# Optimization experiments

Hardware: AMD Instinct MI355X
Metric: run time of the kernel (lower is better)

Reference implementation:

```python
import jax, jax.numpy as jnp
import numpy as np
import math

D_MODEL = 1024
N_HEADS = 16
HEAD_DIM = D_MODEL // N_HEADS


def setup_inputs() -> dict:
    key = jax.random.key(0)
    k1, k2, k3 = jax.random.split(key, 3)
    B, T = 2, 2048
    x = jax.random.normal(k1, (B, T, D_MODEL), dtype=jnp.float32)
    W_qkv = jax.random.normal(k2, (D_MODEL, 3 * D_MODEL), dtype=jnp.float32) * (1.0 / math.sqrt(D_MODEL))
    W_out = jax.random.normal(k3, (D_MODEL, D_MODEL), dtype=jnp.float32) * (1.0 / math.sqrt(D_MODEL))
    return {"x": x, "W_qkv": W_qkv, "W_out": W_out}


def reference(x, W_qkv, W_out):
    B, T, C = x.shape
    qkv = x @ W_qkv  # [B, T, 3C]
    q, k, v = jnp.split(qkv, 3, axis=-1)

    def heads(t):  # [B,T,C] -> [B,H,T,Dh]
        return t.reshape(B, T, N_HEADS, HEAD_DIM).transpose(0, 2, 1, 3)

    q, k, v = heads(q), heads(k), heads(v)
    scale = 1.0 / math.sqrt(HEAD_DIM)
    scores = jnp.einsum('bhtd,bhsd->bhts', q, k) * scale  # [B,H,T,T]
    causal = jnp.tril(jnp.ones((T, T), dtype=bool))
    scores = jnp.where(causal[None, None, :, :], scores, -jnp.inf)
    attn = jax.nn.softmax(scores, axis=-1)
    out = jnp.einsum('bhts,bhsd->bhtd', attn, v)  # [B,H,T,Dh]
    out = out.transpose(0, 2, 1, 3).reshape(B, T, C)
    return out @ W_out
```

## Files before the change

kernel.cpp:

```cpp
#include <hip/hip_runtime.h>
#include <hip/hip_bf16.h>

typedef __bf16 bf16;
typedef bf16 bf16x4 __attribute__((ext_vector_type(4)));
typedef bf16 bf16x8 __attribute__((ext_vector_type(8)));
typedef float f32x4 __attribute__((ext_vector_type(4)));

#define GLOAD16(g, l) __builtin_amdgcn_global_load_lds( \
    (const __attribute__((address_space(1))) void*)(g),  \
    (__attribute__((address_space(3))) void*)(l), 16, 0, 0)

#define EXP2F(x) __builtin_amdgcn_exp2f(x)
#define MFMA16(a, b, c) __builtin_amdgcn_mfma_f32_16x16x32_bf16(a, b, c, 0, 0, 0)

__global__ __launch_bounds__(256) void prep(const float* __restrict__ x,
                                            const float* __restrict__ Wqkv,
                                            const float* __restrict__ Wout,
                                            bf16* __restrict__ xb,
                                            bf16* __restrict__ wqkvT,
                                            bf16* __restrict__ woutT) {
  int id = blockIdx.x, tid = threadIdx.x;
  if (id < 2048) {
    int i = id * 256 + tid;
    const float4* p = (const float4*)x + (size_t)i * 2;
    float4 a = p[0], b = p[1];
    bf16x8 o;
    o[0] = (bf16)a.x; o[1] = (bf16)a.y; o[2] = (bf16)a.z; o[3] = (bf16)a.w;
    o[4] = (bf16)b.x; o[5] = (bf16)b.y; o[6] = (bf16)b.z; o[7] = (bf16)b.w;
    ((bf16x8*)xb)[i] = o;
  } else {
    __shared__ float tile[32][33];
    const float* src; bf16* dst; int N, j;
    if (id < 5120) { src = Wqkv; dst = wqkvT; N = 3072; j = id - 2048; }
    else           { src = Wout; dst = woutT; N = 1024; j = id - 5120; }
    int ntile = N / 32;
    int n0 = (j % ntile) * 32, k0 = (j / ntile) * 32;
    int tx = tid & 31, ty = tid >> 5;
#pragma unroll
    for (int i = 0; i < 4; i++)
      tile[ty + 8 * i][tx] = src[(size_t)(k0 + ty + 8 * i) * N + n0 + tx];
    __syncthreads();
#pragma unroll
    for (int i = 0; i < 4; i++)
      dst[(size_t)(n0 + ty + 8 * i) * 1024 + k0 + tx] = (bf16)tile[tx][ty + 8 * i];
  }
}

__device__ __forceinline__ void gemm_mainloop64(const bf16* __restrict__ A,
                                                const bf16* __restrict__ Bt,
                                                int K, int m0, int n0,
                                                f32x4 acc[4][4],
                                                bf16* As, bf16* Bs) {
  int tid = threadIdx.x;
  int lane = tid & 63;
  int wave = tid >> 6;
  int wr = wave >> 1, wc = wave & 1;
  int c16 = lane & 15, g = lane >> 4;
  f32x4 z = {0.f, 0.f, 0.f, 0.f};
#pragma unroll
  for (int m = 0; m < 4; m++)
#pragma unroll
    for (int n = 0; n < 4; n++) acc[m][n] = z;
  for (int k0 = 0; k0 < K; k0 += 64) {
#pragma unroll
    for (int i = 0; i < 4; i++) {
      int cc = tid + i * 256;
      int r = cc >> 3, ch = cc & 7;
      int sc = ch ^ (r & 7);
      GLOAD16(A + (size_t)(m0 + r) * K + k0 + sc * 8, As + cc * 8);
    }
#pragma unroll
    for (int i = 0; i < 4; i++) {
      int cc = tid + i * 256;
      int r = cc >> 3, ch = cc & 7;
      int sc = ch ^ (r & 7);
      GLOAD16(Bt + (size_t)(n0 + r) * K + k0 + sc * 8, Bs + cc * 8);
    }
    __syncthreads();
#pragma unroll
    for (int h = 0; h < 2; h++) {
      bf16x8 af[4], bfr[4];
#pragma unroll
      for (int m = 0; m < 4; m++) {
        int ar = wr * 64 + m * 16 + c16;
        af[m] = *(const bf16x8*)((const char*)As + ar * 128 + (((h * 4 + g) ^ (ar & 7)) << 4));
      }
#pragma unroll
      for (int n = 0; n < 4; n++) {
        int br = wc * 64 + n * 16 + c16;
        bfr[n] = *(const bf16x8*)((const char*)Bs + br * 128 + (((h * 4 + g) ^ (br & 7)) << 4));
      }
      __builtin_amdgcn_s_setprio(1);
#pragma unroll
      for (int m = 0; m < 4; m++)
#pragma unroll
        for (int n = 0; n < 4; n++)
          acc[m][n] = MFMA16(af[m], bfr[n], acc[m][n]);
      __builtin_amdgcn_s_setprio(0);
    }
    __syncthreads();
  }
}

__global__ __launch_bounds__(256) void gemm_qkv(const bf16* __restrict__ A,
                                                const bf16* __restrict__ Bt,
                                                bf16* __restrict__ q,
                                                bf16* __restrict__ kk,
                                                bf16* __restrict__ vt) {
  __shared__ bf16 As[128 * 64];
  __shared__ bf16 Bs[128 * 64];
  int id = blockIdx.x;
  int xc = id & 7, k = id >> 3;
  int bn = xc * 3 + (k % 3), bm = k / 3;
  int m0 = bm * 128, n0 = bn * 128;
  f32x4 acc[4][4];
  gemm_mainloop64(A, Bt, 1024, m0, n0, acc, As, Bs);
  int lane = threadIdx.x & 63;
  int wave = threadIdx.x >> 6;
  int wr = wave >> 1, wc = wave & 1;
  int c16 = lane & 15, g = lane >> 4;
  int which = n0 >> 10;
  const float QSCALE = 0.125f * 1.4426950408889634f;
  if (which == 2) {
#pragma unroll
    for (int m = 0; m < 4; m++)
#pragma unroll
      for (int n = 0; n < 4; n++) {
        int gm0 = m0 + wr * 64 + m * 16 + g * 4;
        int gn = n0 + wc * 64 + n * 16 + c16;
        int rem = gn & 1023, h = rem >> 6, d = rem & 63;
        int b = gm0 >> 11, t0 = gm0 & 2047;
        size_t bh = (size_t)(b * 16 + h);
        bf16x4 pv;
        pv[0] = (bf16)acc[m][n][0]; pv[1] = (bf16)acc[m][n][1];
        pv[2] = (bf16)acc[m][n][2]; pv[3] = (bf16)acc[m][n][3];
        *(bf16x4*)(vt + (bh * 64 + d) * 2048 + t0) = pv;
      }
  } else {
#pragma unroll
    for (int m = 0; m < 4; m++)
#pragma unroll
      for (int n = 0; n < 4; n++)
#pragma unroll
        for (int j = 0; j < 4; j++) {
          int gm = m0 + wr * 64 + m * 16 + g * 4 + j;
          int gn = n0 + wc * 64 + n * 16 + c16;
          int rem = gn & 1023, h = rem >> 6, d = rem & 63;
          int b = gm >> 11, t = gm & 2047;
          float v = acc[m][n][j];
          size_t bh = (size_t)(b * 16 + h);
          if (which == 0) q[(bh * 2048 + t) * 64 + d]  = (bf16)(v * QSCALE);
          else            kk[(bh * 2048 + t) * 64 + d] = (bf16)v;
        }
  }
}

__global__ __launch_bounds__(256) void gemm_out(const bf16* __restrict__ A,
                                                const bf16* __restrict__ Bt,
                                                float* __restrict__ C) {
  __shared__ bf16 As[64 * 64];
  __shared__ bf16 Bs[128 * 64];
  int tid = threadIdx.x;
  int lane = tid & 63;
  int wave = tid >> 6;
  int wr = wave >> 1, wc = wave & 1;
  int c16 = lane & 15, g = lane >> 4;
  int id = blockIdx.x;
  int bn = id & 7, bm = id >> 3;
  int m0 = bm * 64, n0 = bn * 128;
  const int K = 1024;
  f32x4 acc[2][4];
  {
    f32x4 z = {0.f, 0.f, 0.f, 0.f};
#pragma unroll
    for (int m = 0; m < 2; m++)
#pragma unroll
      for (int n = 0; n < 4; n++) acc[m][n] = z;
  }
  for (int k0 = 0; k0 < K; k0 += 64) {
#pragma unroll
    for (int i = 0; i < 2; i++) {
      int cc = tid + i * 256;
      int r = cc >> 3, ch = cc & 7;
      int sc = ch ^ (r & 7);
      GLOAD16(A + (size_t)(m0 + r) * K + k0 + sc * 8, As + cc * 8);
    }
#pragma unroll
    for (int i = 0; i < 4; i++) {
      int cc = tid + i * 256;
      int r = cc >> 3, ch = cc & 7;
      int sc = ch ^ (r & 7);
      GLOAD16(Bt + (size_t)(n0 + r) * K + k0 + sc * 8, Bs + cc * 8);
    }
    __syncthreads();
#pragma unroll
    for (int h = 0; h < 2; h++) {
      bf16x8 af[2], bfr[4];
#pragma unroll
      for (int m = 0; m < 2; m++) {
        int ar = wr * 32 + m * 16 + c16;
        af[m] = *(const bf16x8*)((const char*)As + ar * 128 + (((h * 4 + g) ^ (ar & 7)) << 4));
      }
#pragma unroll
      for (int n = 0; n < 4; n++) {
        int br = wc * 64 + n * 16 + c16;
        bfr[n] = *(const bf16x8*)((const char*)Bs + br * 128 + (((h * 4 + g) ^ (br & 7)) << 4));
      }
      __builtin_amdgcn_s_setprio(1);
#pragma unroll
      for (int m = 0; m < 2; m++)
#pragma unroll
        for (int n = 0; n < 4; n++)
          acc[m][n] = MFMA16(af[m], bfr[n], acc[m][n]);
      __builtin_amdgcn_s_setprio(0);
    }
    __syncthreads();
  }
#pragma unroll
  for (int m = 0; m < 2; m++)
#pragma unroll
    for (int n = 0; n < 4; n++)
#pragma unroll
      for (int j = 0; j < 4; j++) {
        int gm = m0 + wr * 32 + m * 16 + g * 4 + j;
        int gn = n0 + wc * 64 + n * 16 + c16;
        C[(size_t)gm * 1024 + gn] = acc[m][n][j];
      }
}

__global__ __launch_bounds__(256) void attn(const bf16* __restrict__ q,
                                            const bf16* __restrict__ kk,
                                            const bf16* __restrict__ vt,
                                            bf16* __restrict__ out) {
  __shared__ bf16 Ks[4][64 * 64];
  __shared__ bf16 Vs[4][64 * 64];
  __shared__ bf16 Ps[4 * 32 * 64];
  int tid = threadIdx.x, lane = tid & 63, w = tid >> 6;
  int c16 = lane & 15, g = (lane >> 4) & 3, g4 = g * 4;

  int id = blockIdx.x;
  int c = id & 7;
  int k = id >> 3;
  int s = k >> 5;
  int j5 = k & 31;
  int bxi = j5 & 15, b2 = j5 >> 4;
  int bx = s ? (15 - bxi) : bxi;
  int bh = 4 * c + 2 * b2 + s;
  int q0 = bx * 128;

  const bf16* qb = q  + (size_t)bh * 2048 * 64;
  const bf16* kb = kk + (size_t)bh * 2048 * 64;
  const bf16* vb = vt + (size_t)bh * 64 * 2048;
  int nt = 2 * bx + 2;
  int ns = nt >> 1;

  int qlo = q0 + w * 32;
  bf16x8 qf[2][2];
#pragma unroll
  for (int m = 0; m < 2; m++)
#pragma unroll
    for (int ks = 0; ks < 2; ks++)
      qf[m][ks] = *(const bf16x8*)(qb + (size_t)(qlo + m * 16 + c16) * 64 + ks * 32 + g * 8);
#pragma unroll
  for (int i = 0; i < 2; i++) {
    int cc = tid + i * 256;
    int r = cc >> 3;
    int sw = ((cc & 7) ^ (r & 7)) * 8;
    GLOAD16(kb + (size_t)r * 64 + sw, Ks[0] + cc * 8);
    GLOAD16(vb + (size_t)r * 2048 + sw, Vs[0] + cc * 8);
    GLOAD16(kb + (size_t)(64 + r) * 64 + sw, Ks[1] + cc * 8);
    GLOAD16(vb + (size_t)r * 2048 + 64 + sw, Vs[1] + cc * 8);
  }
  __syncthreads();

  f32x4 o[2][4];
  float lrun[2] = {0.f, 0.f};
  {
    f32x4 z = {0.f, 0.f, 0.f, 0.f};
#pragma unroll
    for (int m = 0; m < 2; m++)
#pragma unroll
      for (int n = 0; n < 4; n++) o[m][n] = z;
  }
  bf16* Pw = Ps + w * 2048;

  for (int st = 0; st < ns; ++st) {
    if (st + 1 < ns) {
      int sn = st * 128 + 128;
      int nb = (2 * st + 2) & 3;
#pragma unroll
      for (int i = 0; i < 2; i++) {
        int cc = tid + i * 256;
        int r = cc >> 3;
        int sw = ((cc & 7) ^ (r & 7)) * 8;
        GLOAD16(kb + (size_t)(sn + r) * 64 + sw, Ks[nb] + cc * 8);
        GLOAD16(vb + (size_t)r * 2048 + sn + sw, Vs[nb] + cc * 8);
        GLOAD16(kb + (size_t)(sn + 64 + r) * 64 + sw, Ks[nb + 1] + cc * 8);
        GLOAD16(vb + (size_t)r * 2048 + sn + 64 + sw, Vs[nb + 1] + cc * 8);
      }
    }
#pragma unroll
    for (int half = 0; half < 2; ++half) {
      int t = 2 * st + half;
      int s0 = t * 64;
      if (s0 > qlo + 31) continue;
      const char* Kb = (const char*)Ks[t & 3];
      const char* Vb = (const char*)Vs[t & 3];
      f32x4 S[2][4];
      {
        f32x4 z = {0.f, 0.f, 0.f, 0.f};
#pragma unroll
        for (int m = 0; m < 2; m++)
#pragma unroll
          for (int n = 0; n < 4; n++) S[m][n] = z;
      }
      __builtin_amdgcn_s_setprio(1);
#pragma unroll
      for (int ks = 0; ks < 2; ks++) {
        bf16x8 kf[4];
#pragma unroll
        for (int n = 0; n < 4; n++) {
          int srow = n * 16 + c16;
          kf[n] = *(const bf16x8*)(Kb + srow * 128 + (((ks * 4 + g) ^ (srow & 7)) << 4));
        }
#pragma unroll
        for (int m = 0; m < 2; m++)
#pragma unroll
          for (int n = 0; n < 4; n++)
            S[m][n] = MFMA16(kf[n], qf[m][ks], S[m][n]);
      }
      __builtin_amdgcn_s_setprio(0);
      bool diag = (s0 + 63 > qlo);
#pragma unroll
      for (int m = 0; m < 2; m++) {
        int qr = qlo + m * 16 + c16;
        if (diag) {
#pragma unroll
          for (int n = 0; n < 4; n++)
#pragma unroll
            for (int rr = 0; rr < 4; rr++)
              if (s0 + n * 16 + g4 + rr > qr) S[m][n][rr] = -__builtin_inff();
        }
        float p[4][4];
        float rs = 0.f;
#pragma unroll
        for (int n = 0; n < 4; n++)
#pragma unroll
          for (int rr = 0; rr < 4; rr++) {
            p[n][rr] = EXP2F(S[m][n][rr]);
            rs += p[n][rr];
          }
        lrun[m] += rs;
        int rp = m * 16 + c16;
#pragma unroll
        for (int n = 0; n < 4; n++) {
          bf16x4 pw;
          pw[0] = (bf16)p[n][0]; pw[1] = (bf16)p[n][1];
          pw[2] = (bf16)p[n][2]; pw[3] = (bf16)p[n][3];
          *(bf16x4*)(Pw + rp * 64 + (((2 * n + (g >> 1)) ^ (c16 & 7)) * 8) + (g & 1) * 4) = pw;
        }
      }
      __builtin_amdgcn_s_setprio(1);
#pragma unroll
      for (int ks = 0; ks < 2; ks++) {
        bf16x8 vf[4];
#pragma unroll
        for (int n = 0; n < 4; n++) {
          int drow = n * 16 + c16;
          vf[n] = *(const bf16x8*)(Vb + drow * 128 + (((ks * 4 + g) ^ (drow & 7)) << 4));
        }
#pragma unroll
        for (int m = 0; m < 2; m++) {
          bf16x8 pf = *(const bf16x8*)(Pw + (m * 16 + c16) * 64 + (((ks * 4 + g) ^ (c16 & 7)) * 8));
#pragma unroll
          for (int n = 0; n < 4; n++)
            o[m][n] = MFMA16(pf, vf[n], o[m][n]);
        }
      }
      __builtin_amdgcn_s_setprio(0);
    }
    if (st + 1 < ns) {
      asm volatile("s_waitcnt vmcnt(0)" ::: "memory");
      __builtin_amdgcn_s_barrier();
      __builtin_amdgcn_sched_barrier(0);
    }
  }
  int b = bh >> 4, h = bh & 15;
#pragma unroll
  for (int m = 0; m < 2; m++) {
    float lm = lrun[m];
    lm += __shfl_xor(lm, 16);
    lm += __shfl_xor(lm, 32);
#pragma unroll
    for (int j = 0; j < 4; j++) {
      float lv = __shfl(lm, (lane & 48) | (g4 + j));
      float inv = 1.f / lv;
      int t = qlo + m * 16 + g4 + j;
#pragma unroll
      for (int n = 0; n < 4; n++) {
        int col = h * 64 + n * 16 + c16;
        out[((size_t)(b * 2048 + t)) * 1024 + col] = (bf16)(o[m][n][j] * inv);
      }
    }
  }
}

extern "C" void kernel_launch(void* const* d_in, const int* in_sizes, int n_in,
                              void* d_out, int out_size, void* d_ws, size_t ws_size,
                              hipStream_t stream) {
  const float* x    = (const float*)d_in[0];
  const float* Wqkv = (const float*)d_in[1];
  const float* Wout = (const float*)d_in[2];
  float* outp = (float*)d_out;
  char* ws = (char*)d_ws;
  const size_t MB = 1024 * 1024;
  bf16* xb    = (bf16*)(ws);
  bf16* wqkvT = (bf16*)(ws + 8 * MB);
  bf16* woutT = (bf16*)(ws + 14 * MB);
  bf16* qb    = (bf16*)(ws + 16 * MB);
  bf16* kb    = (bf16*)(ws + 24 * MB);
  bf16* vtb   = (bf16*)(ws + 32 * MB);

  hipLaunchKernelGGL(prep, dim3(6144), dim3(256), 0, stream,
                     x, Wqkv, Wout, xb, wqkvT, woutT);
  hipLaunchKernelGGL(gemm_qkv, dim3(768), dim3(256), 0, stream,
                     xb, wqkvT, qb, kb, vtb);
  hipLaunchKernelGGL(attn, dim3(512), dim3(256), 0, stream,
                     qb, kb, vtb, xb);
  hipLaunchKernelGGL(gemm_out, dim3(512), dim3(256), 0, stream,
                     xb, woutT, outp);
}
```

Baseline: 103.2 us.

## Use 32x32 MFMA in attention and keep P in registers via permlane swap

Switches the attention kernel from 16x16x32 MFMA tiles to 32x32x16 tiles, laid out so the transposed score accumulator can feed the PV matmul directly. The probabilities are packed to bf16 with v_cvt_pk_bf16_f32 and exchanged across half-waves with v_permlane32_swap, which removes the per-wave LDS staging buffer for P along with its writes and reads. The row-sum reduction is simplified and the output is stored as 4-wide bf16 vectors. The risk is higher register pressure from the 16-wide accumulators, and the new lane mapping has to be correct.

```diff
diff --git a/kernel.cpp b/kernel.cpp
--- a/kernel.cpp
+++ b/kernel.cpp
@@ -5,6 +5,8 @@
 typedef bf16 bf16x4 __attribute__((ext_vector_type(4)));
 typedef bf16 bf16x8 __attribute__((ext_vector_type(8)));
 typedef float f32x4 __attribute__((ext_vector_type(4)));
+typedef float f32x16 __attribute__((ext_vector_type(16)));
+typedef unsigned int u32x4 __attribute__((ext_vector_type(4)));
 
 #define GLOAD16(g, l) __builtin_amdgcn_global_load_lds( \
     (const __attribute__((address_space(1))) void*)(g),  \
@@ -12,6 +14,7 @@
 
 #define EXP2F(x) __builtin_amdgcn_exp2f(x)
 #define MFMA16(a, b, c) __builtin_amdgcn_mfma_f32_16x16x32_bf16(a, b, c, 0, 0, 0)
+#define MFMA32(a, b, c) __builtin_amdgcn_mfma_f32_32x32x16_bf16(a, b, c, 0, 0, 0)
 
 __global__ __launch_bounds__(256) void prep(const float* __restrict__ x,
                                             const float* __restrict__ Wqkv,
@@ -234,9 +237,8 @@
                                             bf16* __restrict__ out) {
   __shared__ bf16 Ks[4][64 * 64];
   __shared__ bf16 Vs[4][64 * 64];
-  __shared__ bf16 Ps[4 * 32 * 64];
   int tid = threadIdx.x, lane = tid & 63, w = tid >> 6;
-  int c16 = lane & 15, g = (lane >> 4) & 3, g4 = g * 4;
+  int ql = lane & 31, hi = lane >> 5;
 
   int id = blockIdx.x;
   int c = id & 7;
@@ -255,12 +257,13 @@
   int ns = nt >> 1;
 
   int qlo = q0 + w * 32;
-  bf16x8 qf[2][2];
-#pragma unroll
-  for (int m = 0; m < 2; m++)
-#pragma unroll
-    for (int ks = 0; ks < 2; ks++)
-      qf[m][ks] = *(const bf16x8*)(qb + (size_t)(qlo + m * 16 + c16) * 64 + ks * 32 + g * 8);
+  int qg = qlo + ql;
+
+  bf16x8 qf[4];
+#pragma unroll
+  for (int j = 0; j < 4; j++)
+    qf[j] = *(const bf16x8*)(qb + (size_t)qg * 64 + j * 16 + hi * 8);
+
 #pragma unroll
   for (int i = 0; i < 2; i++) {
     int cc = tid + i * 256;
@@ -273,16 +276,10 @@
   }
   __syncthreads();
 
-  f32x4 o[2][4];
-  float lrun[2] = {0.f, 0.f};
-  {
-    f32x4 z = {0.f, 0.f, 0.f, 0.f};
-#pragma unroll
-    for (int m = 0; m < 2; m++)
-#pragma unroll
-      for (int n = 0; n < 4; n++) o[m][n] = z;
-  }
-  bf16* Pw = Ps + w * 2048;
+  f32x16 o[2];
+#pragma unroll
+  for (int i = 0; i < 16; i++) { o[0][i] = 0.f; o[1][i] = 0.f; }
+  float lsum = 0.f;
 
   for (int st = 0; st < ns; ++st) {
     if (st + 1 < ns) {
@@ -306,76 +303,54 @@
       if (s0 > qlo + 31) continue;
       const char* Kb = (const char*)Ks[t & 3];
       const char* Vb = (const char*)Vs[t & 3];
-      f32x4 S[2][4];
-      {
-        f32x4 z = {0.f, 0.f, 0.f, 0.f};
-#pragma unroll
-        for (int m = 0; m < 2; m++)
-#pragma unroll
-          for (int n = 0; n < 4; n++) S[m][n] = z;
-      }
+      f32x16 S[2];
+#pragma unroll
+      for (int i = 0; i < 16; i++) { S[0][i] = 0.f; S[1][i] = 0.f; }
       __builtin_amdgcn_s_setprio(1);
 #pragma unroll
-      for (int ks = 0; ks < 2; ks++) {
-        bf16x8 kf[4];
-#pragma unroll
-        for (int n = 0; n < 4; n++) {
-          int srow = n * 16 + c16;
-          kf[n] = *(const bf16x8*)(Kb + srow * 128 + (((ks * 4 + g) ^ (srow & 7)) << 4));
+      for (int j = 0; j < 4; j++) {
+        int row0 = ql, row1 = 32 + ql;
+        bf16x8 kf0 = *(const bf16x8*)(Kb + row0 * 128 + (((2 * j + hi) ^ (row0 & 7)) << 4));
+        bf16x8 kf1 = *(const bf16x8*)(Kb + row1 * 128 + (((2 * j + hi) ^ (row1 & 7)) << 4));
+        S[0] = MFMA32(kf0, qf[j], S[0]);
+        S[1] = MFMA32(kf1, qf[j], S[1]);
+      }
+      __builtin_amdgcn_s_setprio(0);
+      if (s0 + 63 > qlo) {
+#pragma unroll
+        for (int sb = 0; sb < 2; sb++)
+#pragma unroll
+          for (int r = 0; r < 16; r++) {
+            int sg = s0 + sb * 32 + (r & 3) + 8 * (r >> 2) + 4 * hi;
+            if (sg > qg) S[sb][r] = -__builtin_inff();
+          }
+      }
+#pragma unroll
+      for (int sb = 0; sb < 2; sb++)
+#pragma unroll
+        for (int r = 0; r < 16; r++) {
+          float pv2 = EXP2F(S[sb][r]);
+          S[sb][r] = pv2;
+          lsum += pv2;
         }
-#pragma unroll
-        for (int m = 0; m < 2; m++)
-#pragma unroll
-          for (int n = 0; n < 4; n++)
-            S[m][n] = MFMA16(kf[n], qf[m][ks], S[m][n]);
-      }
-      __builtin_amdgcn_s_setprio(0);
-      bool diag = (s0 + 63 > qlo);
-#pragma unroll
-      for (int m = 0; m < 2; m++) {
-        int qr = qlo + m * 16 + c16;
-        if (diag) {
-#pragma unroll
-          for (int n = 0; n < 4; n++)
-#pragma unroll
-            for (int rr = 0; rr < 4; rr++)
-              if (s0 + n * 16 + g4 + rr > qr) S[m][n][rr] = -__builtin_inff();
-        }
-        float p[4][4];
-        float rs = 0.f;
-#pragma unroll
-        for (int n = 0; n < 4; n++)
-#pragma unroll
-          for (int rr = 0; rr < 4; rr++) {
-            p[n][rr] = EXP2F(S[m][n][rr]);
-            rs += p[n][rr];
-          }
-        lrun[m] += rs;
-        int rp = m * 16 + c16;
-#pragma unroll
-        for (int n = 0; n < 4; n++) {
-          bf16x4 pw;
-          pw[0] = (bf16)p[n][0]; pw[1] = (bf16)p[n][1];
-          pw[2] = (bf16)p[n][2]; pw[3] = (bf16)p[n][3];
-          *(bf16x4*)(Pw + rp * 64 + (((2 * n + (g >> 1)) ^ (c16 & 7)) * 8) + (g & 1) * 4) = pw;
-        }
-      }
       __builtin_amdgcn_s_setprio(1);
 #pragma unroll
-      for (int ks = 0; ks < 2; ks++) {
-        bf16x8 vf[4];
-#pragma unroll
-        for (int n = 0; n < 4; n++) {
-          int drow = n * 16 + c16;
-          vf[n] = *(const bf16x8*)(Vb + drow * 128 + (((ks * 4 + g) ^ (drow & 7)) << 4));
-        }
-#pragma unroll
-        for (int m = 0; m < 2; m++) {
-          bf16x8 pf = *(const bf16x8*)(Pw + (m * 16 + c16) * 64 + (((ks * 4 + g) ^ (c16 & 7)) * 8));
-#pragma unroll
-          for (int n = 0; n < 4; n++)
-            o[m][n] = MFMA16(pf, vf[n], o[m][n]);
-        }
+      for (int j = 0; j < 4; j++) {
+        int sb = j >> 1, rb = (j & 1) * 8;
+        unsigned pa, pb, pc, pd;
+        asm("v_cvt_pk_bf16_f32 %0, %1, %2" : "=v"(pa) : "v"(S[sb][rb + 0]), "v"(S[sb][rb + 1]));
+        asm("v_cvt_pk_bf16_f32 %0, %1, %2" : "=v"(pb) : "v"(S[sb][rb + 2]), "v"(S[sb][rb + 3]));
+        asm("v_cvt_pk_bf16_f32 %0, %1, %2" : "=v"(pc) : "v"(S[sb][rb + 4]), "v"(S[sb][rb + 5]));
+        asm("v_cvt_pk_bf16_f32 %0, %1, %2" : "=v"(pd) : "v"(S[sb][rb + 6]), "v"(S[sb][rb + 7]));
+        asm("v_permlane32_swap_b32 %0, %1" : "+v"(pa), "+v"(pc));
+        asm("v_permlane32_swap_b32 %0, %1" : "+v"(pb), "+v"(pd));
+        union { u32x4 u; bf16x8 h; } pu;
+        pu.u[0] = pa; pu.u[1] = pb; pu.u[2] = pc; pu.u[3] = pd;
+        int row0 = ql, row1 = 32 + ql;
+        bf16x8 vf0 = *(const bf16x8*)(Vb + row0 * 128 + (((2 * j + hi) ^ (row0 & 7)) << 4));
+        bf16x8 vf1 = *(const bf16x8*)(Vb + row1 * 128 + (((2 * j + hi) ^ (row1 & 7)) << 4));
+        o[0] = MFMA32(vf0, pu.h, o[0]);
+        o[1] = MFMA32(vf1, pu.h, o[1]);
       }
       __builtin_amdgcn_s_setprio(0);
     }
@@ -385,24 +360,19 @@
       __builtin_amdgcn_sched_barrier(0);
     }
   }
+  lsum += __shfl_xor(lsum, 32);
+  float inv = 1.f / lsum;
   int b = bh >> 4, h = bh & 15;
-#pragma unroll
-  for (int m = 0; m < 2; m++) {
-    float lm = lrun[m];
-    lm += __shfl_xor(lm, 16);
-    lm += __shfl_xor(lm, 32);
-#pragma unroll
-    for (int j = 0; j < 4; j++) {
-      float lv = __shfl(lm, (lane & 48) | (g4 + j));
-      float inv = 1.f / lv;
-      int t = qlo + m * 16 + g4 + j;
-#pragma unroll
-      for (int n = 0; n < 4; n++) {
-        int col = h * 64 + n * 16 + c16;
-        out[((size_t)(b * 2048 + t)) * 1024 + col] = (bf16)(o[m][n][j] * inv);
-      }
-    }
-  }
+  size_t rowbase = ((size_t)(b * 2048 + qg)) * 1024 + h * 64;
+#pragma unroll
+  for (int db = 0; db < 2; db++)
+#pragma unroll
+    for (int qd = 0; qd < 4; qd++) {
+      bf16x4 pv;
+#pragma unroll
+      for (int i = 0; i < 4; i++) pv[i] = (bf16)(o[db][4 * qd + i] * inv);
+      *(bf16x4*)(out + rowbase + db * 32 + 8 * qd + 4 * hi) = pv;
+    }
 }
 
 extern "C" void kernel_launch(void* const* d_in, const int* in_sizes, int n_in,
```

Result: no change. 101.4 us (-1.7%).
